# Performance work log

Hardware: AMD Instinct MI355X
Metric: run time of the kernel (lower is better)

## Reference

```python
import jax, jax.numpy as jnp
import numpy as np

B, N_N, N_A, D = 1024, 96, 96, 512


def _normalize(x):
    return x / jnp.linalg.norm(x, axis=-1, keepdims=True)


def setup_inputs() -> dict:
    key = jax.random.key(0)
    ks = jax.random.split(key, 8)
    img_embs = _normalize(jax.random.normal(ks[0], (B, D), jnp.float32))
    normal_text_embs = _normalize(jax.random.normal(ks[1], (N_N, D), jnp.float32))
    abnormal_text_embs = _normalize(jax.random.normal(ks[2], (N_A, D), jnp.float32))
    logit_scale = jnp.full((1,), np.log(100.0), jnp.float32)  # CLIP temperature
    W1 = jax.random.normal(ks[3], (2 * D, D), jnp.float32) / np.sqrt(2 * D)
    b1 = jnp.zeros((D,), jnp.float32)
    W2 = jax.random.normal(ks[4], (D, D // 2), jnp.float32) / np.sqrt(D)
    b2 = jnp.zeros((D // 2,), jnp.float32)
    W3 = jax.random.normal(ks[5], (D // 2, D // 4), jnp.float32) / np.sqrt(D // 2)
    b3 = jnp.zeros((D // 4,), jnp.float32)
    return {"img_embs": img_embs, "normal_text_embs": normal_text_embs,
            "abnormal_text_embs": abnormal_text_embs, "logit_scale": logit_scale,
            "W1": W1, "b1": b1, "W2": W2, "b2": b2, "W3": W3, "b3": b3}


def _mlp(x, W1, b1, W2, b2, W3, b3):
    h = jax.nn.relu(x @ W1 + b1)
    h = jax.nn.relu(h @ W2 + b2)
    return h @ W3 + b3


def _branch(img_embs, text_embs, scale, W1, b1, W2, b2, W3, b3):
    # sims: [B, N]; softmax weights then exp-scaled text embeddings
    sims = (img_embs @ text_embs.T) * scale
    w = jax.nn.softmax(sims, axis=-1)
    scaled_text = text_embs[None, :, :] * jnp.exp(w)[:, :, None]      # [B, N, D]
    rep_img = jnp.broadcast_to(img_embs[:, None, :], scaled_text.shape)  # [B, N, D]
    x = jnp.concatenate([rep_img, scaled_text], axis=-1)              # [B, N, 2D]
    h = _mlp(x, W1, b1, W2, b2, W3, b3)                               # [B, N, D//4]
    return h.mean(axis=1)                                             # [B, D//4]


def reference(img_embs, normal_text_embs, abnormal_text_embs, logit_scale,
              W1, b1, W2, b2, W3, b3):
    scale = jnp.exp(logit_scale[0])
    h_n = _branch(img_embs, normal_text_embs, scale, W1, b1, W2, b2, W3, b3)
    h_a = _branch(img_embs, abnormal_text_embs, scale, W1, b1, W2, b2, W3, b3)
    return (h_n, h_a)
```

## Files before the change

### kernel.cpp

```cpp
#include <hip/hip_runtime.h>
#include <hip/hip_bf16.h>


typedef __attribute__((ext_vector_type(8))) short short8;
typedef __attribute__((ext_vector_type(4))) float floatx4;
typedef __attribute__((ext_vector_type(2))) float float2v;
typedef __attribute__((ext_vector_type(4))) unsigned int uint4v;

__device__ __forceinline__ unsigned short f2bf(float x) {
    unsigned int u = __float_as_uint(x);
    u += 0x7fffu + ((u >> 16) & 1u);
    return (unsigned short)(u >> 16);
}

template <bool BF16OUT>
__device__ __forceinline__ void gemm32(
    const float* __restrict__ A0, const float* __restrict__ A1, int rows0,
    const float* __restrict__ Bm, float* __restrict__ Cf,
    unsigned short* __restrict__ Cb, int mt, int nt, float* sAT, int t) {
    int r0 = mt * 32, c0 = nt * 64;
    int rg = t >> 4, cg = t & 15;
    int lrow = t >> 3, k4 = (t & 7) * 4;
    int gr = r0 + lrow;
    const float* Ap = (gr < rows0) ? (A0 + gr * 512) : (A1 + (gr - rows0) * 512);
    float acc[2][4];
#pragma unroll
    for (int r = 0; r < 2; r++)
#pragma unroll
        for (int c = 0; c < 4; c++) acc[r][c] = 0.f;
    const float* Bp = Bm + c0 + cg * 4;
    for (int k0 = 0; k0 < 512; k0 += 32) {
        __syncthreads();
        float4 av = *(const float4*)(Ap + k0 + k4);
        sAT[(k4 + 0) * 34 + lrow] = av.x;
        sAT[(k4 + 1) * 34 + lrow] = av.y;
        sAT[(k4 + 2) * 34 + lrow] = av.z;
        sAT[(k4 + 3) * 34 + lrow] = av.w;
        __syncthreads();
#pragma unroll 8
        for (int kk = 0; kk < 32; kk++) {
            float a0 = sAT[kk * 34 + rg * 2];
            float a1 = sAT[kk * 34 + rg * 2 + 1];
            float4 bv = *(const float4*)(Bp + (k0 + kk) * 512);
            acc[0][0] = fmaf(a0, bv.x, acc[0][0]); acc[0][1] = fmaf(a0, bv.y, acc[0][1]);
            acc[0][2] = fmaf(a0, bv.z, acc[0][2]); acc[0][3] = fmaf(a0, bv.w, acc[0][3]);
            acc[1][0] = fmaf(a1, bv.x, acc[1][0]); acc[1][1] = fmaf(a1, bv.y, acc[1][1]);
            acc[1][2] = fmaf(a1, bv.z, acc[1][2]); acc[1][3] = fmaf(a1, bv.w, acc[1][3]);
        }
    }
    int rr = r0 + rg * 2, cc = c0 + cg * 4;
#pragma unroll
    for (int r = 0; r < 2; r++) {
        if (BF16OUT) {
            unsigned long long pk =
                (unsigned long long)f2bf(acc[r][0]) | ((unsigned long long)f2bf(acc[r][1]) << 16) |
                ((unsigned long long)f2bf(acc[r][2]) << 32) | ((unsigned long long)f2bf(acc[r][3]) << 48);
            *(unsigned long long*)(Cb + (rr + r) * 512 + cc) = pk;
        } else {
            *(float4*)(Cf + (rr + r) * 512 + cc) = make_float4(acc[r][0], acc[r][1], acc[r][2], acc[r][3]);
        }
    }
}

__global__ __launch_bounds__(256) void prep_kernel(
    const float* __restrict__ img, const float* __restrict__ tn,
    const float* __restrict__ ta, const float* __restrict__ ls,
    const float* __restrict__ W1, const float* __restrict__ W2,
    float* __restrict__ e_ws, float* __restrict__ U_ws,
    unsigned short* __restrict__ Tb, unsigned short* __restrict__ W2Tf) {
    __shared__ __align__(16) float smem[8704];
    int idx = blockIdx.x;
    int t = threadIdx.x;

    if (idx < 256) {
        int bi0 = idx * 4;
        float* sImg = smem;
        float* sS   = smem + 2064;
        float* sMx  = smem + 2832;
        float* sSum = smem + 2840;
#pragma unroll
        for (int p = 0; p < 2; p++) {
            int i4 = t + 256 * p;
            int i = i4 >> 7, k4 = (i4 & 127) * 4;
            float4 v = *(const float4*)(img + (bi0 + i) * 512 + k4);
            sImg[i * 516 + k4 + 0] = v.x; sImg[i * 516 + k4 + 1] = v.y;
            sImg[i * 516 + k4 + 2] = v.z; sImg[i * 516 + k4 + 3] = v.w;
        }
        __syncthreads();
        float scale = __expf(ls[0]);
        int i = t & 3, n0 = (t >> 2) * 3;
        const float* txp[3];
#pragma unroll
        for (int r = 0; r < 3; r++) {
            int n = n0 + r;
            txp[r] = (n < 96) ? (tn + n * 512) : (ta + (n - 96) * 512);
        }
        float d0 = 0.f, d1 = 0.f, d2 = 0.f;
        const float* ib = &sImg[i * 516];
#pragma unroll 4
        for (int k4 = 0; k4 < 512; k4 += 4) {
            float4 iv = *(const float4*)(ib + k4);
            float4 a = *(const float4*)(txp[0] + k4);
            float4 b = *(const float4*)(txp[1] + k4);
            float4 c = *(const float4*)(txp[2] + k4);
            d0 += iv.x * a.x + iv.y * a.y + iv.z * a.z + iv.w * a.w;
            d1 += iv.x * b.x + iv.y * b.y + iv.z * b.z + iv.w * b.w;
            d2 += iv.x * c.x + iv.y * c.y + iv.z * c.z + iv.w * c.w;
        }
        sS[i * 192 + n0 + 0] = d0 * scale;
        sS[i * 192 + n0 + 1] = d1 * scale;
        sS[i * 192 + n0 + 2] = d2 * scale;
        __syncthreads();
        if (t < 8) {
            int ii = t >> 1, brx = t & 1;
            const float* base = &sS[ii * 192 + brx * 96];
            float m = -1e30f;
            for (int n = 0; n < 96; n++) m = fmaxf(m, base[n]);
            float s = 0.f;
            for (int n = 0; n < 96; n++) s += __expf(base[n] - m);
            sMx[t] = m; sSum[t] = s;
        }
        __syncthreads();
#pragma unroll
        for (int p = 0; p < 3; p++) {
            int j = t + 256 * p;
            int ii = j & 3, n = j >> 2;
            int brx = (n >= 96) ? 1 : 0;
            int nn = n - brx * 96;
            float w = __expf(sS[ii * 192 + n] - sMx[ii * 2 + brx]) / sSum[ii * 2 + brx];
            e_ws[(brx * 1024 + bi0 + ii) * 96 + nn] = __expf(w);
        }
    } else if (idx < 512) {
        int i2 = idx - 256;
        gemm32<false>(img, img, 1 << 20, W1, U_ws, nullptr, i2 >> 3, i2 & 7, smem, t);
    } else if (idx < 560) {
        int i2 = idx - 512;
        gemm32<true>(tn, ta, 96, W1 + 512 * 512, nullptr, Tb, i2 >> 3, i2 & 7, smem, t);
    } else {
        int kt = idx - 560;
        int k0 = kt * 32;
        float* sWT = smem;
        int kr = t >> 3, n0 = (t & 7) * 32;
#pragma unroll
        for (int c = 0; c < 8; c++) {
            float4 v = *(const float4*)(W2 + (k0 + kr) * 256 + n0 + c * 4);
            sWT[(n0 + c * 4 + 0) * 33 + kr] = v.x;
            sWT[(n0 + c * 4 + 1) * 33 + kr] = v.y;
            sWT[(n0 + c * 4 + 2) * 33 + kr] = v.z;
            sWT[(n0 + c * 4 + 3) * 33 + kr] = v.w;
        }
        __syncthreads();
        int lane = t & 63;
        int kl = (lane >> 4) * 8;
#pragma unroll
        for (int it = 0; it < 4; it++) {
            int nt = it * 4 + (t >> 6);
            int n = nt * 16 + (lane & 15);
            uint4v u;
#pragma unroll
            for (int c = 0; c < 4; c++) {
                unsigned short lo = f2bf(sWT[n * 33 + kl + 2 * c]);
                unsigned short hi = f2bf(sWT[n * 33 + kl + 2 * c + 1]);
                u[c] = (unsigned int)lo | ((unsigned int)hi << 16);
            }
            *(uint4v*)(W2Tf + (((kt * 16 + nt) * 64) + lane) * 8) = u;
        }
    }
}

__device__ __forceinline__ uint4v stage8(float ev, short8 tv, const float2v* u2) {
    uint4v tp; __builtin_memcpy(&tp, &tv, 16);
    float2v e2 = {ev, ev};
    const float2v z2 = {0.f, 0.f};
    uint4v pk;
#pragma unroll
    for (int jj = 0; jj < 4; jj++) {
        float2v t2;
        t2.x = __uint_as_float(tp[jj] << 16);
        t2.y = __uint_as_float(tp[jj] & 0xffff0000u);
        float2v f = __builtin_elementwise_fma(e2, t2, u2[jj]);
        f = __builtin_elementwise_max(f, z2);
        __hip_bfloat162 h2 = __float22bfloat162_rn(make_float2(f.x, f.y));
        unsigned int bits; __builtin_memcpy(&bits, &h2, 4);
        pk[jj] = bits;
    }
    return pk;
}

__global__ __launch_bounds__(512, 4) void branch_mlp11(
    const float* __restrict__ U, const unsigned short* __restrict__ Tb,
    const float* __restrict__ e_all, const unsigned short* __restrict__ W2Tf,
    const float* __restrict__ b1, const float* __restrict__ b2,
    const float* __restrict__ W3, const float* __restrict__ b3,
    float* __restrict__ out) {
    int b = blockIdx.x, br = blockIdx.y;
    const unsigned short* T = Tb + br * (96 * 512);

    __shared__ float sUb[512];
    __shared__ float sE[96];
    __shared__ __align__(16) unsigned short sH[2][96 * 64];
    __shared__ float sM2[256];
    __shared__ float sPart[512];

    int t = threadIdx.x;
    sUb[t] = U[b * 512 + t] + b1[t];
    if (t < 96) sE[t] = e_all[(br * 1024 + b) * 96 + t];

    const int wave = t >> 6, lane = t & 63;
    const int frow = lane & 15, fkq = (lane >> 4) * 8;
    const int f7 = frow & 7;
    const bool two = (t < 256);
    const int srowA = two ? (t >> 3) : (64 + ((t - 256) >> 3));
    const int srowB = two ? (srowA + 32) : srowA;
    const int skc = (t & 7) * 8;
    const int sw = skc ^ ((srowA & 7) * 8);
    const int ka0 = (((fkq >> 3) ^ f7) << 3);
    const int ka1 = (((4 + (fkq >> 3)) ^ f7) << 3);

    const floatx4 fz = {0.f, 0.f, 0.f, 0.f};
    floatx4 acc[6][2];
#pragma unroll
    for (int mt = 0; mt < 6; mt++) {
        acc[mt][0] = fz; acc[mt][1] = fz;
    }

    short8 tvA = *(const short8*)(T + srowA * 512 + skc);
    short8 tvB = *(const short8*)(T + srowB * 512 + skc);
    const unsigned short* Wf = W2Tf + (wave * 2 * 64 + lane) * 8;

    __syncthreads();

    float evA = sE[srowA];
    float evB = sE[srowB];

    {
        float2v u2[4];
#pragma unroll
        for (int jj = 0; jj < 4; jj++) u2[jj] = *(const float2v*)(&sUb[skc + 2 * jj]);
        *(uint4v*)(&sH[0][srowA * 64 + sw]) = stage8(evA, tvA, u2);
        if (two) *(uint4v*)(&sH[0][srowB * 64 + sw]) = stage8(evB, tvB, u2);
    }

#pragma unroll
    for (int s = 0; s < 8; s++) {
        int k0 = s * 64;
        unsigned short* sHb = sH[s & 1];
        __syncthreads();

        short8 b0f[2], b1f[2];
#pragma unroll
        for (int j = 0; j < 2; j++)
            b0f[j] = *(const short8*)(Wf + ((2 * s) * 16 + j) * 512);
#pragma unroll
        for (int j = 0; j < 2; j++)
            b1f[j] = *(const short8*)(Wf + ((2 * s + 1) * 16 + j) * 512);
        if (s < 7) {
            tvA = *(const short8*)(T + srowA * 512 + k0 + 64 + skc);
            tvB = *(const short8*)(T + srowB * 512 + k0 + 64 + skc);
        }

#pragma unroll
        for (int mt = 0; mt < 6; mt++) {
            short8 afr = *(const short8*)(&sHb[(mt * 16 + frow) * 64 + ka0]);
            acc[mt][0] = __builtin_amdgcn_mfma_f32_16x16x32_bf16(afr, b0f[0], acc[mt][0], 0, 0, 0);
            acc[mt][1] = __builtin_amdgcn_mfma_f32_16x16x32_bf16(afr, b0f[1], acc[mt][1], 0, 0, 0);
        }
#pragma unroll
        for (int mt = 0; mt < 6; mt++) {
            short8 afr = *(const short8*)(&sHb[(mt * 16 + frow) * 64 + ka1]);
            acc[mt][0] = __builtin_amdgcn_mfma_f32_16x16x32_bf16(afr, b1f[0], acc[mt][0], 0, 0, 0);
            acc[mt][1] = __builtin_amdgcn_mfma_f32_16x16x32_bf16(afr, b1f[1], acc[mt][1], 0, 0, 0);
        }

        if (s < 7) {
            unsigned short* sHn = sH[(s + 1) & 1];
            float2v u2[4];
#pragma unroll
            for (int jj = 0; jj < 4; jj++)
                u2[jj] = *(const float2v*)(&sUb[k0 + 64 + skc + 2 * jj]);
            *(uint4v*)(&sHn[srowA * 64 + sw]) = stage8(evA, tvA, u2);
            if (two) *(uint4v*)(&sHn[srowB * 64 + sw]) = stage8(evB, tvB, u2);
        }
    }

#pragma unroll
    for (int j = 0; j < 2; j++) {
        int col = wave * 32 + j * 16 + frow;
        float bb = b2[col];
        float s = 0.f;
#pragma unroll
        for (int mt = 0; mt < 6; mt++)
#pragma unroll
            for (int r = 0; r < 4; r++)
                s += fmaxf(acc[mt][j][r] + bb, 0.f);
        s += __shfl_xor(s, 16);
        s += __shfl_xor(s, 32);
        if (lane < 16) sM2[col] = s * (1.0f / 96.0f);
    }
    __syncthreads();

    int col = t & 127, kq = t >> 7;
    const float* w3p = W3 + (kq * 64) * 128 + col;
    const float* mp = sM2 + kq * 64;
    float o = 0.f;
#pragma unroll 8
    for (int k = 0; k < 64; k++) o = fmaf(mp[k], w3p[k * 128], o);
    sPart[t] = o;
    __syncthreads();
    if (t < 128)
        out[(br * 1024 + b) * 128 + t] =
            sPart[t] + sPart[t + 128] + sPart[t + 256] + sPart[t + 384] + b3[t];
}

extern "C" void kernel_launch(void* const* d_in, const int* in_sizes, int n_in,
                              void* d_out, int out_size, void* d_ws, size_t ws_size,
                              hipStream_t stream) {
    const float* img = (const float*)d_in[0];
    const float* tn  = (const float*)d_in[1];
    const float* ta  = (const float*)d_in[2];
    const float* ls  = (const float*)d_in[3];
    const float* W1  = (const float*)d_in[4];
    const float* b1  = (const float*)d_in[5];
    const float* W2  = (const float*)d_in[6];
    const float* b2  = (const float*)d_in[7];
    const float* W3  = (const float*)d_in[8];
    const float* b3  = (const float*)d_in[9];
    float* out = (float*)d_out;
    float* ws  = (float*)d_ws;

    float* e_ws = ws;
    float* U_ws = ws + 196608;
    unsigned short* Tb   = (unsigned short*)(ws + 720896);
    unsigned short* W2Tf = (unsigned short*)(ws + 770048);

    prep_kernel<<<576, 256, 0, stream>>>(img, tn, ta, ls, W1, W2, e_ws, U_ws, Tb, W2Tf);
    branch_mlp11<<<dim3(1024, 2), 512, 0, stream>>>(U_ws, Tb, e_ws, W2Tf, b1, b2, W3, b3, out);
}
```

Baseline: 177.5 us.

## Split waves into 2x4 row/column tiles and prefetch next W2 fragments

Remaps the 8 waves from 1x8 column slices (96 rows x 32 cols each) to a 2x4 grid (48 rows x 64 cols each). Each A fragment read from shared memory now feeds four MFMAs instead of two, so LDS reads per wave are halved. The first half of the next stage's W2 fragments is prefetched into registers one iteration ahead. In exchange, a partial-sum buffer and an extra barrier are needed to combine the two row halves for the mean, and register pressure rises.

Measured after the change: 194.4 us. 9.5% more time.

```diff
diff --git a/kernel.cpp b/kernel.cpp
--- a/kernel.cpp
+++ b/kernel.cpp
@@ -187,7 +187,7 @@
     return pk;
 }
 
-__global__ __launch_bounds__(512, 4) void branch_mlp11(
+__global__ __launch_bounds__(512, 4) void branch_mlp12(
     const float* __restrict__ U, const unsigned short* __restrict__ Tb,
     const float* __restrict__ e_all, const unsigned short* __restrict__ W2Tf,
     const float* __restrict__ b1, const float* __restrict__ b2,
@@ -199,6 +199,7 @@
     __shared__ float sUb[512];
     __shared__ float sE[96];
     __shared__ __align__(16) unsigned short sH[2][96 * 64];
+    __shared__ float sM2p[512];
     __shared__ float sM2[256];
     __shared__ float sPart[512];
 
@@ -207,31 +208,36 @@
     if (t < 96) sE[t] = e_all[(br * 1024 + b) * 96 + t];
 
     const int wave = t >> 6, lane = t & 63;
+    const int cg4 = wave & 3, rh = wave >> 2;
     const int frow = lane & 15, fkq = (lane >> 4) * 8;
     const int f7 = frow & 7;
     const bool two = (t < 256);
     const int srowA = two ? (t >> 3) : (64 + ((t - 256) >> 3));
-    const int srowB = two ? (srowA + 32) : srowA;
+    const int srowB = srowA + 32;
     const int skc = (t & 7) * 8;
     const int sw = skc ^ ((srowA & 7) * 8);
     const int ka0 = (((fkq >> 3) ^ f7) << 3);
     const int ka1 = (((4 + (fkq >> 3)) ^ f7) << 3);
 
     const floatx4 fz = {0.f, 0.f, 0.f, 0.f};
-    floatx4 acc[6][2];
-#pragma unroll
-    for (int mt = 0; mt < 6; mt++) {
-        acc[mt][0] = fz; acc[mt][1] = fz;
-    }
+    floatx4 acc[3][4];
+#pragma unroll
+    for (int mt = 0; mt < 3; mt++)
+#pragma unroll
+        for (int j = 0; j < 4; j++) acc[mt][j] = fz;
 
     short8 tvA = *(const short8*)(T + srowA * 512 + skc);
-    short8 tvB = *(const short8*)(T + srowB * 512 + skc);
-    const unsigned short* Wf = W2Tf + (wave * 2 * 64 + lane) * 8;
+    short8 tvB = two ? *(const short8*)(T + srowB * 512 + skc) : tvA;
+    const unsigned short* Wf = W2Tf + (cg4 * 4 * 64 + lane) * 8;
+    short8 bpre[4];
+#pragma unroll
+    for (int j = 0; j < 4; j++)
+        bpre[j] = *(const short8*)(Wf + j * 512);
 
     __syncthreads();
 
     float evA = sE[srowA];
-    float evB = sE[srowB];
+    float evB = two ? sE[srowB] : 0.f;
 
     {
         float2v u2[4];
@@ -247,30 +253,37 @@
         unsigned short* sHb = sH[s & 1];
         __syncthreads();
 
-        short8 b0f[2], b1f[2];
-#pragma unroll
-        for (int j = 0; j < 2; j++)
-            b0f[j] = *(const short8*)(Wf + ((2 * s) * 16 + j) * 512);
-#pragma unroll
-        for (int j = 0; j < 2; j++)
+        short8 b1f[4];
+#pragma unroll
+        for (int j = 0; j < 4; j++)
             b1f[j] = *(const short8*)(Wf + ((2 * s + 1) * 16 + j) * 512);
         if (s < 7) {
             tvA = *(const short8*)(T + srowA * 512 + k0 + 64 + skc);
-            tvB = *(const short8*)(T + srowB * 512 + k0 + 64 + skc);
-        }
-
-#pragma unroll
-        for (int mt = 0; mt < 6; mt++) {
-            short8 afr = *(const short8*)(&sHb[(mt * 16 + frow) * 64 + ka0]);
-            acc[mt][0] = __builtin_amdgcn_mfma_f32_16x16x32_bf16(afr, b0f[0], acc[mt][0], 0, 0, 0);
-            acc[mt][1] = __builtin_amdgcn_mfma_f32_16x16x32_bf16(afr, b0f[1], acc[mt][1], 0, 0, 0);
-        }
-#pragma unroll
-        for (int mt = 0; mt < 6; mt++) {
-            short8 afr = *(const short8*)(&sHb[(mt * 16 + frow) * 64 + ka1]);
-            acc[mt][0] = __builtin_amdgcn_mfma_f32_16x16x32_bf16(afr, b1f[0], acc[mt][0], 0, 0, 0);
-            acc[mt][1] = __builtin_amdgcn_mfma_f32_16x16x32_bf16(afr, b1f[1], acc[mt][1], 0, 0, 0);
-        }
+            if (two) tvB = *(const short8*)(T + srowB * 512 + k0 + 64 + skc);
+        }
+        short8 bnext[4];
+        if (s < 7) {
+#pragma unroll
+            for (int j = 0; j < 4; j++)
+                bnext[j] = *(const short8*)(Wf + ((2 * s + 2) * 16 + j) * 512);
+        }
+
+#pragma unroll
+        for (int mt = 0; mt < 3; mt++) {
+            short8 afr = *(const short8*)(&sHb[((rh * 48 + mt * 16 + frow) * 64) + ka0]);
+#pragma unroll
+            for (int j = 0; j < 4; j++)
+                acc[mt][j] = __builtin_amdgcn_mfma_f32_16x16x32_bf16(afr, bpre[j], acc[mt][j], 0, 0, 0);
+        }
+#pragma unroll
+        for (int mt = 0; mt < 3; mt++) {
+            short8 afr = *(const short8*)(&sHb[((rh * 48 + mt * 16 + frow) * 64) + ka1]);
+#pragma unroll
+            for (int j = 0; j < 4; j++)
+                acc[mt][j] = __builtin_amdgcn_mfma_f32_16x16x32_bf16(afr, b1f[j], acc[mt][j], 0, 0, 0);
+        }
+#pragma unroll
+        for (int j = 0; j < 4; j++) bpre[j] = bnext[j];
 
         if (s < 7) {
             unsigned short* sHn = sH[(s + 1) & 1];
@@ -284,19 +297,21 @@
     }
 
 #pragma unroll
-    for (int j = 0; j < 2; j++) {
-        int col = wave * 32 + j * 16 + frow;
+    for (int j = 0; j < 4; j++) {
+        int col = cg4 * 64 + j * 16 + frow;
         float bb = b2[col];
         float s = 0.f;
 #pragma unroll
-        for (int mt = 0; mt < 6; mt++)
+        for (int mt = 0; mt < 3; mt++)
 #pragma unroll
             for (int r = 0; r < 4; r++)
                 s += fmaxf(acc[mt][j][r] + bb, 0.f);
         s += __shfl_xor(s, 16);
         s += __shfl_xor(s, 32);
-        if (lane < 16) sM2[col] = s * (1.0f / 96.0f);
-    }
+        if (lane < 16) sM2p[rh * 256 + col] = s;
+    }
+    __syncthreads();
+    if (t < 256) sM2[t] = (sM2p[t] + sM2p[256 + t]) * (1.0f / 96.0f);
     __syncthreads();
 
     int col = t & 127, kq = t >> 7;
@@ -334,5 +349,5 @@
     unsigned short* W2Tf = (unsigned short*)(ws + 770048);
 
     prep_kernel<<<576, 256, 0, stream>>>(img, tn, ta, ls, W1, W2, e_ws, U_ws, Tb, W2Tf);
-    branch_mlp11<<<dim3(1024, 2), 512, 0, stream>>>(U_ws, Tb, e_ws, W2Tf, b1, b2, W3, b3, out);
-}
+    branch_mlp12<<<dim3(1024, 2), 512, 0, stream>>>(U_ws, Tb, e_ws, W2Tf, b1, b2, W3, b3, out);
+}
```
